# Kernel tuning notes

Measured on AMD Instinct MI355X. Metric: run time of the kernel, lower is better.

The kernel has to match this reference:

```python
import jax, jax.numpy as jnp
import numpy as np

B, N, K = 8, 2048, 16   # batch, points, neighbors (after dropping self)
EPS = 1e-5


def _bn(y, g, b, m, v):
    # eval-mode batchnorm over channel dim 1, y: [B,C,...]
    sh = (1, -1) + (1,) * (y.ndim - 2)
    inv = g.reshape(sh) / jnp.sqrt(v.reshape(sh) + EPS)
    return (y - m.reshape(sh)) * inv + b.reshape(sh)


def setup_inputs() -> dict:
    key = jax.random.key(0)
    ks = jax.random.split(key, 16)
    d = {}
    d["x"] = jax.random.normal(ks[0], (B, 3, N), dtype=jnp.float32)
    # pre: Conv1d(3->24, k=1) + BN
    d["w_pre"] = jax.random.normal(ks[1], (24, 3), dtype=jnp.float32) * 0.3
    d["b_pre"] = jax.random.normal(ks[2], (24,), dtype=jnp.float32) * 0.1
    d["g_pre"] = 1.0 + 0.1 * jax.random.normal(ks[3], (24,), dtype=jnp.float32)
    d["be_pre"] = 0.1 * jax.random.normal(ks[4], (24,), dtype=jnp.float32)
    d["m_pre"] = 0.1 * jax.random.normal(ks[5], (24,), dtype=jnp.float32)
    d["v_pre"] = jax.random.uniform(ks[6], (24,), minval=0.5, maxval=1.5, dtype=jnp.float32)
    # shared_mlp_1: Conv2d(48->12, 1, bias=False) + BN
    d["w1"] = jax.random.normal(ks[7], (12, 48), dtype=jnp.float32) * 0.15
    d["g1"] = 1.0 + 0.1 * jax.random.normal(ks[8], (12,), dtype=jnp.float32)
    d["be1"] = 0.1 * jax.random.normal(ks[9], (12,), dtype=jnp.float32)
    d["m1"] = 0.1 * jax.random.normal(ks[10], (12,), dtype=jnp.float32)
    d["v1"] = jax.random.uniform(ks[11], (12,), minval=0.5, maxval=1.5, dtype=jnp.float32)
    # shared_mlp_2: Conv2d(60->12, 1, bias=False) + BN
    d["w2"] = jax.random.normal(ks[12], (12, 60), dtype=jnp.float32) * 0.15
    d["g2"] = 1.0 + 0.1 * jax.random.normal(ks[13], (12,), dtype=jnp.float32)
    d["be2"] = 0.1 * jax.random.normal(ks[14], (12,), dtype=jnp.float32)
    d["m2"] = 0.1 * jax.random.normal(ks[15], (12,), dtype=jnp.float32)
    d["v2"] = jnp.ones((12,), dtype=jnp.float32)
    # shared_mlp_3: Conv2d(72->12, 1, bias=False), no BN
    d["w3"] = jax.random.normal(jax.random.fold_in(key, 99), (12, 72), dtype=jnp.float32) * 0.15
    return d


def reference(x, w_pre, b_pre, g_pre, be_pre, m_pre, v_pre,
              w1, g1, be1, m1, v1, w2, g2, be2, m2, v2, w3):
    # pre: 1x1 conv1d + BN + ReLU -> [B,24,N]
    pre = jnp.einsum('oc,bcn->bon', w_pre, x) + b_pre[None, :, None]
    pre = jax.nn.relu(_bn(pre, g_pre, be_pre, m_pre, v_pre))

    # kNN on xyz = x.detach(): [B,N,3]
    pts = jax.lax.stop_gradient(jnp.swapaxes(x, 1, 2))
    sq = jnp.sum(pts * pts, axis=-1)                              # [B,N]
    d2 = sq[:, :, None] + sq[:, None, :] - 2.0 * jnp.einsum('bnc,bmc->bnm', pts, pts)
    _, idx = jax.lax.top_k(-d2, K + 1)                             # nearest K+1 incl. self
    idx = idx[..., 1:]                                             # drop self -> [B,N,K]

    # gather neighbor features: [B,24,N,K]
    grouped = jax.vmap(lambda f, i: f[:, i])(pre, idx)
    center = jnp.broadcast_to(pre[..., None], grouped.shape)
    y = jnp.concatenate([center, grouped], axis=1)                 # [B,48,N,K]

    h1 = jax.nn.relu(_bn(jnp.einsum('oc,bcnk->bonk', w1, y), g1, be1, m1, v1))
    y = jnp.concatenate([h1, y], axis=1)                           # [B,60,N,K]
    h2 = jax.nn.relu(_bn(jnp.einsum('oc,bcnk->bonk', w2, y), g2, be2, m2, v2))
    y = jnp.concatenate([h2, y], axis=1)                           # [B,72,N,K]
    h3 = jnp.einsum('oc,bcnk->bonk', w3, y)
    y = jnp.concatenate([h3, y], axis=1)                           # [B,84,N,K]

    y = jnp.max(y, axis=-1)                                        # maxpool over neighbors -> [B,84,N]
    return jnp.concatenate([y, x], axis=1)                         # [B,87,N]
```

## Files before the change

### kernel.cpp

```cpp
#include <hip/hip_runtime.h>
#include <math.h>

#define EPS 1e-5f
#define NBATCH 8
#define NPTS 2048
#define KNB 16
#define BIG 3.2e38f

#define CHUNK_PTS 16
#define KNN_BLKS (NBATCH * 128)
#define FUSED_LDS 40960

#define WS_PRE 0
#define WS_AUX (16384 * 24)
#define WS_IDX (WS_AUX + 16384 * 72)

__device__ __forceinline__ float dist2f(float mex, float mey, float mez,
                                        float sqn, float4 q) {
  float dot2 = fmaf(mex, q.x, fmaf(mey, q.y, __fmul_rn(mez, q.z)));
  return __fsub_rn(__fadd_rn(sqn, q.w), dot2);
}

__global__ __launch_bounds__(512, 8) void fused_kernel(
    const float* __restrict__ x,
    const float* __restrict__ w_pre, const float* __restrict__ b_pre,
    const float* __restrict__ g_pre, const float* __restrict__ be_pre,
    const float* __restrict__ m_pre, const float* __restrict__ v_pre,
    const float* __restrict__ w1, const float* __restrict__ g1,
    const float* __restrict__ be1, const float* __restrict__ m1,
    const float* __restrict__ v1,
    const float* __restrict__ w2, const float* __restrict__ g2,
    const float* __restrict__ be2, const float* __restrict__ m2,
    const float* __restrict__ v2, const float* __restrict__ w3,
    float* __restrict__ pre, float* __restrict__ aux,
    int* __restrict__ knn_out) {
  extern __shared__ char smem[];
  float4* C4   = (float4*)smem;
  float* slist = (float*)(smem + 32768);
  float* fwp   = slist;
  float* fbp   = fwp + 72;
  float* fw1t  = fbp + 24;
  float* fb1   = fw1t + 576;
  float* fw2t  = fb1 + 12;
  float* fb2   = fw2t + 720;
  float* fw3t  = fb2 + 12;
  float* sinv1 = fw3t + 576;
  float* sinv2 = sinv1 + 12;
  float* sinvP = sinv2 + 12;
  float* sd2  = slist;
  int*   sidx = (int*)(slist + 320);
  int*   scnt = (int*)(slist + 640);

  int tid = threadIdx.x;
  int bi = blockIdx.x;
  int b = bi >> 7, chunk = bi & 127;
  const float* xb = x + (size_t)b * 3 * NPTS;

  for (int j = tid; j < NPTS; j += 512) {
    float xx = xb[j], yy = xb[NPTS + j], zz = xb[2 * NPTS + j];
    float sq = __fadd_rn(__fadd_rn(__fmul_rn(xx, xx), __fmul_rn(yy, yy)),
                         __fmul_rn(zz, zz));
    C4[j] = make_float4(2.0f * xx, 2.0f * yy, 2.0f * zz, sq);
  }
  if (tid < 24) sinvP[tid] = g_pre[tid] / sqrtf(v_pre[tid] + EPS);
  if (tid < 12) { sinv1[tid] = g1[tid] / sqrtf(v1[tid] + EPS);
                  sinv2[tid] = g2[tid] / sqrtf(v2[tid] + EPS); }
  __syncthreads();
  if (tid < 72) fwp[tid] = w_pre[tid] * sinvP[tid / 3];
  if (tid < 24) fbp[tid] = (b_pre[tid] - m_pre[tid]) * sinvP[tid] + be_pre[tid];
  if (tid < 12) { fb1[tid] = be1[tid] - m1[tid] * sinv1[tid];
                  fb2[tid] = be2[tid] - m2[tid] * sinv2[tid]; }
  for (int j = tid; j < 576; j += 512) { int i = j / 12, o = j - i * 12; fw1t[j] = w1[o * 48 + i] * sinv1[o]; }
  for (int j = tid; j < 720; j += 512) { int i = j / 12, o = j - i * 12; fw2t[j] = w2[o * 60 + i] * sinv2[o]; }
  for (int j = tid; j < 576; j += 512) { int i = j / 12, o = j - i * 12; fw3t[j] = w3[o * 72 + 24 + i]; }
  __syncthreads();

  {
    int rr = tid & 31, pt = tid >> 5;
    int n0 = chunk * CHUNK_PTS + pt;
    size_t pgl = (size_t)(b << 11) + n0;
    float x0 = xb[n0], x1 = xb[NPTS + n0], x2 = xb[2 * NPTS + n0];
    float pr[24];
#pragma unroll
    for (int c = 0; c < 24; ++c) {
      float v = fmaf(fwp[c * 3 + 0], x0,
                fmaf(fwp[c * 3 + 1], x1,
                fmaf(fwp[c * 3 + 2], x2, fbp[c])));
      pr[c] = fmaxf(v, 0.f);
    }
    if (rr == 16) {
      float4* o4 = (float4*)(pre + pgl * 24);
#pragma unroll
      for (int i = 0; i < 6; ++i)
        o4[i] = make_float4(pr[4*i], pr[4*i+1], pr[4*i+2], pr[4*i+3]);
    }
    if (rr < 12) {
      int o = rr;
      float u1 = fb1[o], a1 = 0.f, u2 = fb2[o], a2 = 0.f, u3 = 0.f, a3 = 0.f;
#pragma unroll
      for (int i = 0; i < 24; ++i) {
        u1 = fmaf(fw1t[i * 12 + o],        pr[i], u1);
        a1 = fmaf(fw1t[(24 + i) * 12 + o], pr[i], a1);
        u2 = fmaf(fw2t[(12 + i) * 12 + o], pr[i], u2);
        a2 = fmaf(fw2t[(36 + i) * 12 + o], pr[i], a2);
        u3 = fmaf(fw3t[i * 12 + o],        pr[i], u3);
        a3 = fmaf(fw3t[(24 + i) * 12 + o], pr[i], a3);
      }
      float* A = aux + pgl * 72;
      A[o] = u1; A[12 + o] = u2; A[24 + o] = u3;
      A[36 + o] = a1; A[48 + o] = a2; A[60 + o] = a3;
    }
  }
  __syncthreads();

  int p = tid & 15, s = tid >> 4;
  int n = chunk * CHUNK_PTS + p;
  float4 me4 = C4[n];
  float mex = 0.5f * me4.x, mey = 0.5f * me4.y, mez = 0.5f * me4.z;
  float sqn = me4.w;
  const float4* Cs = C4 + s * 64;
  int selfc = n - s * 64;
  float L[16];
#pragma unroll
  for (int t = 0; t < 16; ++t) L[t] = BIG;
  for (int c0 = 0; c0 < 64; c0 += 16) {
    float S[16];
#pragma unroll
    for (int cc = 0; cc < 16; ++cc) {
      float4 q = Cs[c0 + cc];
      float d2 = dist2f(mex, mey, mez, sqn, q);
      S[cc] = ((c0 + cc) == selfc) ? BIG : d2;
    }
#pragma unroll
    for (int pw = 1; pw < 16; pw <<= 1) {
#pragma unroll
      for (int k = pw; k >= 1; k >>= 1) {
#pragma unroll
        for (int j = (k & (pw - 1)); j + k < 16; j += 2 * k) {
#pragma unroll
          for (int i = 0; i < k; ++i) {
            int a = i + j, bq = i + j + k;
            if (bq < 16 && (a / (2 * pw) == bq / (2 * pw))) {
              float lo = fminf(S[a], S[bq]);
              float hi = fmaxf(S[a], S[bq]);
              S[a] = lo; S[bq] = hi;
            }
          }
        }
      }
    }
    float m[16];
#pragma unroll
    for (int i = 0; i < 16; ++i) m[i] = fminf(L[i], S[15 - i]);
#pragma unroll
    for (int d = 8; d >= 1; d >>= 1) {
#pragma unroll
      for (int i = 0; i < 16; ++i) {
        if (!(i & d)) {
          float lo = fminf(m[i], m[i | d]);
          float hi = fmaxf(m[i], m[i | d]);
          m[i] = lo; m[i | d] = hi;
        }
      }
    }
#pragma unroll
    for (int i = 0; i < 16; ++i) L[i] = m[i];
  }
  {
    float bb[16], m16[16];
#pragma unroll
    for (int i = 0; i < 16; ++i) bb[i] = __shfl_xor(L[i], 16, 64);
#pragma unroll
    for (int i = 0; i < 16; ++i) m16[i] = fminf(L[i], bb[15 - i]);
#pragma unroll
    for (int d = 8; d >= 1; d >>= 1) {
#pragma unroll
      for (int i = 0; i < 16; ++i) {
        if (!(i & d)) {
          float lo = fminf(m16[i], m16[i | d]);
          float hi = fmaxf(m16[i], m16[i | d]);
          m16[i] = lo; m16[i | d] = hi;
        }
      }
    }
#pragma unroll
    for (int i = 0; i < 16; ++i) bb[i] = __shfl_xor(m16[i], 32, 64);
    float m2_[16];
#pragma unroll
    for (int i = 0; i < 16; ++i) m2_[i] = fminf(m16[i], bb[15 - i]);
#pragma unroll
    for (int d = 8; d >= 1; d >>= 1) {
#pragma unroll
      for (int i = 0; i < 16; ++i) {
        if (!(i & d)) {
          float lo = fminf(m2_[i], m2_[i | d]);
          float hi = fmaxf(m2_[i], m2_[i | d]);
          m2_[i] = lo; m2_[i | d] = hi;
        }
      }
    }
    if ((s & 3) == 0) {
#pragma unroll
      for (int i = 0; i < 16; ++i) slist[((s >> 2) * 16 + i) * 16 + p] = m2_[i];
    }
  }
  __syncthreads();
  for (int W = 4; W >= 1; W >>= 1) {
    int w = tid >> 4;
    bool act = (w < W);
    float a[16], bb[16];
    if (act) {
#pragma unroll
      for (int i = 0; i < 16; ++i) a[i]  = slist[((2 * w) * 16 + i) * 16 + p];
#pragma unroll
      for (int i = 0; i < 16; ++i) bb[i] = slist[((2 * w + 1) * 16 + i) * 16 + p];
    }
    __syncthreads();
    if (act) {
      float m16[16];
#pragma unroll
      for (int i = 0; i < 16; ++i) m16[i] = fminf(a[i], bb[15 - i]);
#pragma unroll
      for (int d = 8; d >= 1; d >>= 1) {
#pragma unroll
        for (int i = 0; i < 16; ++i) {
          if (!(i & d)) {
            float lo = fminf(m16[i], m16[i | d]);
            float hi = fmaxf(m16[i], m16[i | d]);
            m16[i] = lo; m16[i | d] = hi;
          }
        }
      }
#pragma unroll
      for (int i = 0; i < 16; ++i) slist[(w * 16 + i) * 16 + p] = m16[i];
    }
    __syncthreads();
  }
  float tau = slist[15 * 16 + p];
  __syncthreads();
  for (int j = tid; j < 16 * 20; j += 512) sidx[j] = 0;
  if (tid < 16) scnt[tid] = 0;
  __syncthreads();
#pragma unroll 4
  for (int c = 0; c < 64; ++c) {
    float4 q = Cs[c];
    float d2 = dist2f(mex, mey, mez, sqn, q);
    int j = s * 64 + c;
    if (d2 <= tau && j != n) {
      int pos = atomicAdd(&scnt[p], 1);
      if (pos < 20) { sd2[p * 20 + pos] = d2; sidx[p * 20 + pos] = j; }
    }
  }
  __syncthreads();
  if (tid < 16) {
    int c = scnt[tid]; if (c > 20) c = 20;
    if (c > 16) {
      for (int t = 0; t < 16; ++t) {
        int best = t;
        for (int u = t + 1; u < c; ++u) {
          float da = sd2[tid * 20 + u], db = sd2[tid * 20 + best];
          int ia = sidx[tid * 20 + u], ib = sidx[tid * 20 + best];
          if (da < db || (da == db && ia < ib)) best = u;
        }
        float td = sd2[tid * 20 + t]; sd2[tid * 20 + t] = sd2[tid * 20 + best]; sd2[tid * 20 + best] = td;
        int ti = sidx[tid * 20 + t]; sidx[tid * 20 + t] = sidx[tid * 20 + best]; sidx[tid * 20 + best] = ti;
      }
    }
  }
  __syncthreads();
  if (tid < 256) {
    int pp = tid >> 4, kk = tid & 15;
    knn_out[((size_t)b * NPTS + chunk * CHUNK_PTS + pp) * KNB + kk] = sidx[pp * 20 + kk];
  }
}

__global__ __launch_bounds__(256) void mlp_kernel(
    const float* __restrict__ pre, const float* __restrict__ aux,
    const int* __restrict__ knn, const float* __restrict__ x,
    const float* __restrict__ w2, const float* __restrict__ g2,
    const float* __restrict__ v2, const float* __restrict__ w3,
    float* __restrict__ out) {
  __shared__ float sW2h[144], sW3h2[144], sW3h1[144];
  __shared__ float sout[87 * 16];
  int tid = threadIdx.x;
  if (tid < 144) {
    int o = tid / 12, i = tid - o * 12;
    float inv2 = g2[o] / sqrtf(v2[o] + EPS);
    sW2h[tid]  = w2[o * 60 + i] * inv2;
    sW3h2[tid] = w3[o * 72 + i];
    sW3h1[tid] = w3[o * 72 + 12 + i];
  }
  __syncthreads();
  int k = tid & 15, pl = tid >> 4;
  int p = blockIdx.x * 16 + pl;
  int b = p >> 11, n = p & (NPTS - 1);
  int nb = knn[(size_t)p * KNB + k];
  const float4* u4 = (const float4*)(aux + (size_t)p * 72);
  const float4* a4 = (const float4*)(aux + ((size_t)(b << 11) + nb) * 72 + 36);
  float uc[36], av[36];
#pragma unroll
  for (int i = 0; i < 9; ++i) {
    float4 t = u4[i];
    uc[4*i] = t.x; uc[4*i+1] = t.y; uc[4*i+2] = t.z; uc[4*i+3] = t.w;
    float4 t2 = a4[i];
    av[4*i] = t2.x; av[4*i+1] = t2.y; av[4*i+2] = t2.z; av[4*i+3] = t2.w;
  }
  float h1[12], h2[12], h3[12];
#pragma unroll
  for (int o = 0; o < 12; ++o) h1[o] = fmaxf(uc[o] + av[o], 0.f);
#pragma unroll
  for (int o = 0; o < 12; ++o) {
    float a = uc[12 + o] + av[12 + o];
#pragma unroll
    for (int i = 0; i < 12; ++i) a = fmaf(sW2h[o * 12 + i], h1[i], a);
    h2[o] = fmaxf(a, 0.f);
  }
#pragma unroll
  for (int o = 0; o < 12; ++o) {
    float a = uc[24 + o] + av[24 + o];
#pragma unroll
    for (int i = 0; i < 12; ++i) a = fmaf(sW3h2[o * 12 + i], h2[i], a);
#pragma unroll
    for (int i = 0; i < 12; ++i) a = fmaf(sW3h1[o * 12 + i], h1[i], a);
    h3[o] = a;
  }
  float nbf[24];
  const float4* pn4 = (const float4*)(pre + ((size_t)(b << 11) + nb) * 24);
#pragma unroll
  for (int i = 0; i < 6; ++i) {
    float4 t = pn4[i];
    nbf[4*i] = t.x; nbf[4*i+1] = t.y; nbf[4*i+2] = t.z; nbf[4*i+3] = t.w;
  }
#pragma unroll
  for (int m = 1; m < 16; m <<= 1) {
#pragma unroll
    for (int o = 0; o < 12; ++o) {
      h1[o] = fmaxf(h1[o], __shfl_xor(h1[o], m, 16));
      h2[o] = fmaxf(h2[o], __shfl_xor(h2[o], m, 16));
      h3[o] = fmaxf(h3[o], __shfl_xor(h3[o], m, 16));
    }
#pragma unroll
    for (int i = 0; i < 24; ++i)
      nbf[i] = fmaxf(nbf[i], __shfl_xor(nbf[i], m, 16));
  }
  if (k == 0) {
    const float4* c4 = (const float4*)(pre + (size_t)p * 24);
#pragma unroll
    for (int o = 0; o < 12; ++o) {
      sout[(0  + o) * 16 + pl] = h3[o];
      sout[(12 + o) * 16 + pl] = h2[o];
      sout[(24 + o) * 16 + pl] = h1[o];
    }
#pragma unroll
    for (int i = 0; i < 6; ++i) {
      float4 t = c4[i];
      sout[(36 + 4*i    ) * 16 + pl] = t.x;
      sout[(36 + 4*i + 1) * 16 + pl] = t.y;
      sout[(36 + 4*i + 2) * 16 + pl] = t.z;
      sout[(36 + 4*i + 3) * 16 + pl] = t.w;
    }
#pragma unroll
    for (int i = 0; i < 24; ++i) sout[(60 + i) * 16 + pl] = nbf[i];
    const float* xb = x + (size_t)b * 3 * NPTS + n;
    sout[84 * 16 + pl] = xb[0];
    sout[85 * 16 + pl] = xb[NPTS];
    sout[86 * 16 + pl] = xb[2 * NPTS];
  }
  __syncthreads();
  int n0 = (blockIdx.x * 16) & (NPTS - 1);
  float* ob = out + (size_t)b * 87 * NPTS;
  for (int j2 = tid; j2 < 87 * 16; j2 += 256) {
    int c = j2 >> 4, i = j2 & 15;
    ob[(size_t)c * NPTS + n0 + i] = sout[j2];
  }
}

extern "C" void kernel_launch(void* const* d_in, const int* in_sizes, int n_in,
                              void* d_out, int out_size, void* d_ws, size_t ws_size,
                              hipStream_t stream) {
  (void)in_sizes; (void)n_in; (void)out_size; (void)ws_size;
  const float* x     = (const float*)d_in[0];
  const float* w_pre = (const float*)d_in[1];
  const float* b_pre = (const float*)d_in[2];
  const float* g_pre = (const float*)d_in[3];
  const float* be_pre= (const float*)d_in[4];
  const float* m_pre = (const float*)d_in[5];
  const float* v_pre = (const float*)d_in[6];
  const float* w1    = (const float*)d_in[7];
  const float* g1    = (const float*)d_in[8];
  const float* be1   = (const float*)d_in[9];
  const float* m1    = (const float*)d_in[10];
  const float* v1    = (const float*)d_in[11];
  const float* w2    = (const float*)d_in[12];
  const float* g2    = (const float*)d_in[13];
  const float* be2   = (const float*)d_in[14];
  const float* m2    = (const float*)d_in[15];
  const float* v2    = (const float*)d_in[16];
  const float* w3    = (const float*)d_in[17];
  float* ws  = (float*)d_ws;
  float* pre = ws + WS_PRE;
  float* aux = ws + WS_AUX;
  int*   knn = (int*)(ws + WS_IDX);
  float* out = (float*)d_out;

  fused_kernel<<<KNN_BLKS, 512, FUSED_LDS, stream>>>(
      x, w_pre, b_pre, g_pre, be_pre, m_pre, v_pre,
      w1, g1, be1, m1, v1, w2, g2, be2, m2, v2, w3,
      pre, aux, knn);
  mlp_kernel<<<NBATCH * NPTS / 16, 256, 0, stream>>>(pre, aux, knn, x,
                                                     w2, g2, v2, w3, out);
}
```

Baseline: 155.7 us.

## Process 32 points per block with 1024 threads and shuffle-based top-k merges

Doubles the points handled per fused block, from 16 to 32, using 1024 threads. The per-block staging of all 2048 candidate coordinates and folded weights is now shared by twice as many query points, and the grid is halved. The k-NN merge tree is reorganised so the two 32-lane halves of each wave merge through cross-lane shuffles before the LDS tree reduction. An XOR rotation of candidate order by segment parity is added, apparently to spread LDS bank accesses. In exchange, LDS use rises to 64KB per block and the 1024-thread launch bound tightens the register budget, which risks spills in the register-heavy sorting networks and lower occupancy.

```diff
diff --git a/kernel.cpp b/kernel.cpp
--- a/kernel.cpp
+++ b/kernel.cpp
@@ -7,9 +7,10 @@
 #define KNB 16
 #define BIG 3.2e38f
 
-#define CHUNK_PTS 16
-#define KNN_BLKS (NBATCH * 128)
-#define FUSED_LDS 40960
+#define CHUNK_PTS 32
+#define KNN_BLKS (NBATCH * 64)
+#define THREADS 1024
+#define FUSED_LDS 65536
 
 #define WS_PRE 0
 #define WS_AUX (16384 * 24)
@@ -21,7 +22,7 @@
   return __fsub_rn(__fadd_rn(sqn, q.w), dot2);
 }
 
-__global__ __launch_bounds__(512, 8) void fused_kernel(
+__global__ __launch_bounds__(THREADS, 8) void fused_kernel(
     const float* __restrict__ x,
     const float* __restrict__ w_pre, const float* __restrict__ b_pre,
     const float* __restrict__ g_pre, const float* __restrict__ be_pre,
@@ -48,15 +49,15 @@
   float* sinv2 = sinv1 + 12;
   float* sinvP = sinv2 + 12;
   float* sd2  = slist;
-  int*   sidx = (int*)(slist + 320);
-  int*   scnt = (int*)(slist + 640);
+  int*   sidx = (int*)(slist + 640);
+  int*   scnt = (int*)(slist + 1280);
 
   int tid = threadIdx.x;
   int bi = blockIdx.x;
-  int b = bi >> 7, chunk = bi & 127;
+  int b = bi >> 6, chunk = bi & 63;
   const float* xb = x + (size_t)b * 3 * NPTS;
 
-  for (int j = tid; j < NPTS; j += 512) {
+  for (int j = tid; j < NPTS; j += THREADS) {
     float xx = xb[j], yy = xb[NPTS + j], zz = xb[2 * NPTS + j];
     float sq = __fadd_rn(__fadd_rn(__fmul_rn(xx, xx), __fmul_rn(yy, yy)),
                          __fmul_rn(zz, zz));
@@ -70,9 +71,9 @@
   if (tid < 24) fbp[tid] = (b_pre[tid] - m_pre[tid]) * sinvP[tid] + be_pre[tid];
   if (tid < 12) { fb1[tid] = be1[tid] - m1[tid] * sinv1[tid];
                   fb2[tid] = be2[tid] - m2[tid] * sinv2[tid]; }
-  for (int j = tid; j < 576; j += 512) { int i = j / 12, o = j - i * 12; fw1t[j] = w1[o * 48 + i] * sinv1[o]; }
-  for (int j = tid; j < 720; j += 512) { int i = j / 12, o = j - i * 12; fw2t[j] = w2[o * 60 + i] * sinv2[o]; }
-  for (int j = tid; j < 576; j += 512) { int i = j / 12, o = j - i * 12; fw3t[j] = w3[o * 72 + 24 + i]; }
+  if (tid < 576) { int i = tid / 12, o = tid - i * 12; fw1t[tid] = w1[o * 48 + i] * sinv1[o]; }
+  if (tid < 720) { int i = tid / 12, o = tid - i * 12; fw2t[tid] = w2[o * 60 + i] * sinv2[o]; }
+  if (tid < 576) { int i = tid / 12, o = tid - i * 12; fw3t[tid] = w3[o * 72 + 24 + i]; }
   __syncthreads();
 
   {
@@ -113,13 +114,14 @@
   }
   __syncthreads();
 
-  int p = tid & 15, s = tid >> 4;
+  int p = tid & 31, s = tid >> 5;
   int n = chunk * CHUNK_PTS + p;
   float4 me4 = C4[n];
   float mex = 0.5f * me4.x, mey = 0.5f * me4.y, mez = 0.5f * me4.z;
   float sqn = me4.w;
   const float4* Cs = C4 + s * 64;
   int selfc = n - s * 64;
+  int rot = (s & 1) << 2;
   float L[16];
 #pragma unroll
   for (int t = 0; t < 16; ++t) L[t] = BIG;
@@ -127,9 +129,10 @@
     float S[16];
 #pragma unroll
     for (int cc = 0; cc < 16; ++cc) {
-      float4 q = Cs[c0 + cc];
+      int c2 = (c0 + cc) ^ rot;
+      float4 q = Cs[c2];
       float d2 = dist2f(mex, mey, mez, sqn, q);
-      S[cc] = ((c0 + cc) == selfc) ? BIG : d2;
+      S[cc] = (c2 == selfc) ? BIG : d2;
     }
 #pragma unroll
     for (int pw = 1; pw < 16; pw <<= 1) {
@@ -169,7 +172,7 @@
   {
     float bb[16], m16[16];
 #pragma unroll
-    for (int i = 0; i < 16; ++i) bb[i] = __shfl_xor(L[i], 16, 64);
+    for (int i = 0; i < 16; ++i) bb[i] = __shfl_xor(L[i], 32, 64);
 #pragma unroll
     for (int i = 0; i < 16; ++i) m16[i] = fminf(L[i], bb[15 - i]);
 #pragma unroll
@@ -183,43 +186,29 @@
         }
       }
     }
-#pragma unroll
-    for (int i = 0; i < 16; ++i) bb[i] = __shfl_xor(m16[i], 32, 64);
-    float m2_[16];
-#pragma unroll
-    for (int i = 0; i < 16; ++i) m2_[i] = fminf(m16[i], bb[15 - i]);
-#pragma unroll
-    for (int d = 8; d >= 1; d >>= 1) {
-#pragma unroll
-      for (int i = 0; i < 16; ++i) {
-        if (!(i & d)) {
-          float lo = fminf(m2_[i], m2_[i | d]);
-          float hi = fmaxf(m2_[i], m2_[i | d]);
-          m2_[i] = lo; m2_[i | d] = hi;
-        }
-      }
-    }
-    if ((s & 3) == 0) {
-#pragma unroll
-      for (int i = 0; i < 16; ++i) slist[((s >> 2) * 16 + i) * 16 + p] = m2_[i];
-    }
-  }
-  __syncthreads();
-  for (int W = 4; W >= 1; W >>= 1) {
-    int w = tid >> 4;
+    int w = tid >> 6;
+    if (!(s & 1)) {
+#pragma unroll
+      for (int i = 0; i < 16; ++i) slist[(w * 16 + i) * 32 + p] = m16[i];
+    }
+  }
+  __syncthreads();
+  for (int W = 8; W >= 1; W >>= 1) {
+    int w = tid >> 6;
+    int h = (tid >> 5) & 1;
     bool act = (w < W);
-    float a[16], bb[16];
+    float val[16];
     if (act) {
 #pragma unroll
-      for (int i = 0; i < 16; ++i) a[i]  = slist[((2 * w) * 16 + i) * 16 + p];
-#pragma unroll
-      for (int i = 0; i < 16; ++i) bb[i] = slist[((2 * w + 1) * 16 + i) * 16 + p];
+      for (int i = 0; i < 16; ++i) val[i] = slist[((2 * w + h) * 16 + i) * 32 + p];
     }
     __syncthreads();
     if (act) {
-      float m16[16];
-#pragma unroll
-      for (int i = 0; i < 16; ++i) m16[i] = fminf(a[i], bb[15 - i]);
+      float bb[16], m16[16];
+#pragma unroll
+      for (int i = 0; i < 16; ++i) bb[i] = __shfl_xor(val[i], 32, 64);
+#pragma unroll
+      for (int i = 0; i < 16; ++i) m16[i] = fminf(val[i], bb[15 - i]);
 #pragma unroll
       for (int d = 8; d >= 1; d >>= 1) {
 #pragma unroll
@@ -231,28 +220,31 @@
           }
         }
       }
-#pragma unroll
-      for (int i = 0; i < 16; ++i) slist[(w * 16 + i) * 16 + p] = m16[i];
+      if (h == 0) {
+#pragma unroll
+        for (int i = 0; i < 16; ++i) slist[(w * 16 + i) * 32 + p] = m16[i];
+      }
     }
     __syncthreads();
   }
-  float tau = slist[15 * 16 + p];
-  __syncthreads();
-  for (int j = tid; j < 16 * 20; j += 512) sidx[j] = 0;
-  if (tid < 16) scnt[tid] = 0;
+  float tau = slist[15 * 32 + p];
+  __syncthreads();
+  for (int j = tid; j < 32 * 20; j += THREADS) sidx[j] = 0;
+  if (tid < 32) scnt[tid] = 0;
   __syncthreads();
 #pragma unroll 4
   for (int c = 0; c < 64; ++c) {
-    float4 q = Cs[c];
+    int c2 = c ^ rot;
+    float4 q = Cs[c2];
     float d2 = dist2f(mex, mey, mez, sqn, q);
-    int j = s * 64 + c;
+    int j = s * 64 + c2;
     if (d2 <= tau && j != n) {
       int pos = atomicAdd(&scnt[p], 1);
       if (pos < 20) { sd2[p * 20 + pos] = d2; sidx[p * 20 + pos] = j; }
     }
   }
   __syncthreads();
-  if (tid < 16) {
+  if (tid < 32) {
     int c = scnt[tid]; if (c > 20) c = 20;
     if (c > 16) {
       for (int t = 0; t < 16; ++t) {
@@ -268,7 +260,7 @@
     }
   }
   __syncthreads();
-  if (tid < 256) {
+  if (tid < 512) {
     int pp = tid >> 4, kk = tid & 15;
     knn_out[((size_t)b * NPTS + chunk * CHUNK_PTS + pp) * KNB + kk] = sidx[pp * 20 + kk];
   }
@@ -403,7 +395,7 @@
   int*   knn = (int*)(ws + WS_IDX);
   float* out = (float*)d_out;
 
-  fused_kernel<<<KNN_BLKS, 512, FUSED_LDS, stream>>>(
+  fused_kernel<<<KNN_BLKS, THREADS, FUSED_LDS, stream>>>(
       x, w_pre, b_pre, g_pre, be_pre, m_pre, v_pre,
       w1, g1, be1, m1, v1, w2, g2, be2, m2, v2, w3,
       pre, aux, knn);
```

New measurement: 155.0 us. No clear change (-0.5%).
